# Performance work log

Measured on AMD Instinct MI355X. Metric: run time of the kernel, lower is better.

The kernel has to match this reference:

```python
import jax, jax.numpy as jnp
import numpy as np

N = 50000   # nodes
E = 800000  # edges (avg degree 16)
D = 96      # feature dim (in = hidden = out)


def setup_inputs() -> dict:
    key = jax.random.key(0)
    ks = jax.random.split(key, 6)
    scale = 1.0 / np.sqrt(D)
    return {
        "x": jax.random.normal(ks[0], (N, D), jnp.float32),
        "edge_index": jax.random.randint(ks[1], (2, E), 0, N, dtype=jnp.int64),
        "W1": jax.random.normal(ks[2], (D, D), jnp.float32) * scale,
        "b1": jnp.zeros((D,), jnp.float32),
        "a1": jnp.full((1,), 0.25, jnp.float32),  # PReLU weight
        "W2": jax.random.normal(ks[3], (D, D), jnp.float32) * scale,
        "b2": jnp.zeros((D,), jnp.float32),
    }


def _gcn_conv(x, W, b, src, dst, norm, n):
    # GCNConv: linear transform, then degree-normalized scatter-add aggregation
    h = x @ W                               # [N, D_out]
    msg = h[src] * norm[:, None]            # gather + scale, [E+N, D_out]
    out = jax.ops.segment_sum(msg, dst, num_segments=n)
    return out + b


def reference(x, edge_index, W1, b1, a1, W2, b2):
    n = x.shape[0]
    # add self loops (PyG gcn_norm default, fill_value=1.0)
    loop = jnp.arange(n, dtype=edge_index.dtype)
    src = jnp.concatenate([edge_index[0], loop])
    dst = jnp.concatenate([edge_index[1], loop])
    # symmetric normalization: D^{-1/2} A D^{-1/2}
    ones = jnp.ones(src.shape[0], dtype=x.dtype)
    deg = jax.ops.segment_sum(ones, dst, num_segments=n)
    dinv = jnp.where(deg > 0, jax.lax.rsqrt(deg), 0.0)
    norm = dinv[src] * dinv[dst]

    h = _gcn_conv(x, W1, b1, src, dst, norm, n)
    h = jnp.where(h > 0, h, a1 * h)  # PReLU (dropout p=0.0 is a no-op)
    h = _gcn_conv(h, W2, b2, src, dst, norm, n)
    return h
```

## Files before the change

kernel.cpp:

```cpp
#include <hip/hip_runtime.h>
#include <hip/hip_bf16.h>

#define NNODES 50000
#define NEDGES 800000
#define DIM    96
#define NBUCK  196
#define CAP    4608
#define TM     64
#define XPAD   104
#define PCH    3125

typedef __attribute__((ext_vector_type(8))) short   short8;
typedef __attribute__((ext_vector_type(4))) float   float4v;

__device__ __forceinline__ float loadF(const void* p, long i, int isbf) {
    return isbf ? __bfloat162float(((const __hip_bfloat16*)p)[i])
                : ((const float*)p)[i];
}
__device__ __forceinline__ int clampN(int v) {
    return v < 0 ? 0 : (v >= NNODES ? NNODES - 1 : v);
}
__device__ __forceinline__ int edgeDst(const int* w, int e, int is64) {
    return clampN(is64 ? w[2 * (NEDGES + e)] : w[NEDGES + e]);
}
__device__ __forceinline__ int edgeSrc(const int* w, int e, int is64) {
    return clampN(is64 ? w[2 * e] : w[e]);
}

__global__ void k_sniff(const unsigned* __restrict__ xw,
                        const unsigned* __restrict__ ew,
                        int* __restrict__ flags,
                        int* __restrict__ bcur) {
    int lane = threadIdx.x;
    for (int i = lane; i < NBUCK; i += 64) bcur[i] = 0;
    int bad = 0, nz = 0;
    for (int r = 0; r < 4; ++r) {
        unsigned w  = xw[lane + 64 * r];
        unsigned lo = w & 0xffffu;
        unsigned ex = (lo >> 7) & 0xffu;
        if (!(lo == 0u || (ex >= 90u && ex <= 145u))) bad++;
        unsigned o = ew[2 * (lane + 64 * r) + 1];
        if (o != 0u) nz++;
    }
    for (int off = 32; off; off >>= 1) {
        bad += __shfl_down(bad, off);
        nz  += __shfl_down(nz,  off);
    }
    if (lane == 0) {
        flags[0] = (bad <= 32) ? 1 : 0;
        flags[1] = (nz  <  4) ? 1 : 0;
    }
}

__global__ __launch_bounds__(256) void k_part(const int* __restrict__ w,
                                              int* __restrict__ bcur,
                                              unsigned* __restrict__ ebuf,
                                              const int* __restrict__ flags) {
    __shared__ unsigned pack[PCH];
    __shared__ int h[NBUCK];
    __shared__ int base[NBUCK];
    const int is64 = flags[1];
    const int tid  = threadIdx.x;
    const int e0   = blockIdx.x * PCH;

    for (int i = tid; i < NBUCK; i += 256) h[i] = 0;
    __syncthreads();
    for (int k = tid; k < PCH; k += 256) {
        int e = e0 + k;
        int s = edgeSrc(w, e, is64);
        int d = edgeDst(w, e, is64);
        pack[k] = ((unsigned)d << 16) | (unsigned)s;
        atomicAdd(&h[d >> 8], 1);
    }
    __syncthreads();
    for (int i = tid; i < NBUCK; i += 256) {
        int c = h[i];
        base[i] = c ? i * CAP + atomicAdd(&bcur[i], c) : 0;
        h[i] = 0;
    }
    __syncthreads();
    for (int k = tid; k < PCH; k += 256) {
        unsigned r = pack[k];
        int b = r >> 24;
        int pos = base[b] + atomicAdd(&h[b], 1);
        if (pos < (b + 1) * CAP) ebuf[pos] = r;
    }
}

__global__ __launch_bounds__(512) void k_csr(const unsigned* __restrict__ ebuf,
                                             const int* __restrict__ bcur,
                                             int* __restrict__ rowbeg,
                                             int* __restrict__ rowend,
                                             unsigned short* __restrict__ col,
                                             float* __restrict__ dinv) {
    __shared__ int h256[256];
    __shared__ int sc[256];
    __shared__ int cur[256];
    const int b   = blockIdx.x;
    const int tid = threadIdx.x;
    int cnt = bcur[b]; if (cnt > CAP) cnt = CAP;
    const int e0 = b * CAP;
    const int e1 = e0 + cnt;

    if (tid < 256) h256[tid] = 0;
    __syncthreads();
    for (int e = e0 + tid; e < e1; e += 512)
        atomicAdd(&h256[(ebuf[e] >> 16) & 255], 1);
    __syncthreads();
    int v = 0;
    if (tid < 256) { v = h256[tid]; sc[tid] = v; }
    __syncthreads();
    for (int off = 1; off < 256; off <<= 1) {
        int t2 = 0;
        if (tid < 256 && tid >= off) t2 = sc[tid - off];
        __syncthreads();
        if (tid < 256) sc[tid] += t2;
        __syncthreads();
    }
    if (tid < 256) {
        int start = e0 + sc[tid] - v;
        cur[tid] = start;
        int node = b * 256 + tid;
        if (node < NNODES) {
            rowbeg[node] = start;
            rowend[node] = start + v;
            dinv[node] = rsqrtf((float)v + 1.0f);
        }
    }
    __syncthreads();
    for (int e = e0 + tid; e < e1; e += 512) {
        unsigned r = ebuf[e];
        int pos = atomicAdd(&cur[(r >> 16) & 255], 1);
        col[pos] = (unsigned short)(r & 0xffffu);
    }
}

__global__ __launch_bounds__(256) void k_gemm_mfma(
        const void* __restrict__ X, int x_force_bf16,
        const void* __restrict__ W,
        const float* __restrict__ dinv,
        __hip_bfloat16* __restrict__ g,
        const int* __restrict__ flags) {
    __shared__ __hip_bfloat16 Xs[TM * XPAD];
    __shared__ __hip_bfloat16 Wt[DIM * XPAD];

    const int t    = threadIdx.x;
    const int fbf  = flags[0];
    const int xbf  = x_force_bf16 ? 1 : fbf;
    const int row0 = blockIdx.x * TM;

    if (!fbf) {
        const float4* Wv = (const float4*)W;
        for (int idx = t; idx < DIM * DIM / 4; idx += 256) {
            int k = idx / (DIM / 4);
            int n = (idx - k * (DIM / 4)) * 4;
            float4 w4 = Wv[idx];
            Wt[(n + 0) * XPAD + k] = __float2bfloat16(w4.x);
            Wt[(n + 1) * XPAD + k] = __float2bfloat16(w4.y);
            Wt[(n + 2) * XPAD + k] = __float2bfloat16(w4.z);
            Wt[(n + 3) * XPAD + k] = __float2bfloat16(w4.w);
        }
    } else {
        for (int idx = t; idx < DIM * DIM; idx += 256) {
            int k = idx / DIM, n = idx - k * DIM;
            Wt[n * XPAD + k] = __float2bfloat16(loadF(W, idx, 1));
        }
    }
    if (!xbf) {
        const float4* Xv = (const float4*)X;
        for (int idx = t; idx < TM * (DIM / 4); idx += 256) {
            int r = idx / (DIM / 4);
            int c = (idx - r * (DIM / 4)) * 4;
            int gr = row0 + r;
            float4 vv = {0.f, 0.f, 0.f, 0.f};
            if (gr < NNODES) vv = Xv[(size_t)gr * (DIM / 4) + (c >> 2)];
            *(__hip_bfloat162*)&Xs[r * XPAD + c] =
                __halves2bfloat162(__float2bfloat16(vv.x), __float2bfloat16(vv.y));
            *(__hip_bfloat162*)&Xs[r * XPAD + c + 2] =
                __halves2bfloat162(__float2bfloat16(vv.z), __float2bfloat16(vv.w));
        }
    } else {
        const short* Xs16 = (const short*)X;
        for (int idx = t; idx < TM * (DIM / 8); idx += 256) {
            int r  = idx / (DIM / 8);
            int c8 = idx - r * (DIM / 8);
            int gr = row0 + r;
            short8 vv = {0, 0, 0, 0, 0, 0, 0, 0};
            if (gr < NNODES) vv = *(const short8*)(Xs16 + (size_t)gr * DIM + c8 * 8);
            *(short8*)((short*)Xs + r * XPAD + c8 * 8) = vv;
        }
    }
    __syncthreads();

    const int wave = t >> 6;
    const int lane = t & 63;
    const int m    = lane & 15;
    const int quad = lane >> 4;

    const short* xsp = (const short*)Xs;
    short8 a[3];
#pragma unroll
    for (int kt = 0; kt < 3; ++kt)
        a[kt] = *(const short8*)(xsp + (wave * 16 + m) * XPAD + kt * 32 + quad * 8);

    float dv[4];
#pragma unroll
    for (int r2 = 0; r2 < 4; ++r2) {
        int gr = row0 + wave * 16 + quad * 4 + r2;
        dv[r2] = (gr < NNODES) ? dinv[gr] : 0.f;
    }

    const short* wtp = (const short*)Wt;
#pragma unroll
    for (int nt = 0; nt < 6; ++nt) {
        float4v acc = {0.f, 0.f, 0.f, 0.f};
#pragma unroll
        for (int kt = 0; kt < 3; ++kt) {
            short8 b = *(const short8*)(wtp + (nt * 16 + m) * XPAD + kt * 32 + quad * 8);
            acc = __builtin_amdgcn_mfma_f32_16x16x32_bf16(a[kt], b, acc, 0, 0, 0);
        }
#pragma unroll
        for (int r2 = 0; r2 < 4; ++r2) {
            int gr = row0 + wave * 16 + quad * 4 + r2;
            if (gr < NNODES)
                g[(size_t)gr * DIM + nt * 16 + m] = __float2bfloat16(acc[r2] * dv[r2]);
        }
    }
}

__global__ __launch_bounds__(256) void k_aggr(
        const __hip_bfloat16* __restrict__ g,
        const int* __restrict__ rowbeg,
        const int* __restrict__ rowend,
        const unsigned short* __restrict__ col,
        const float* __restrict__ dinv,
        const void* __restrict__ b,
        const void* __restrict__ a1,
        void* __restrict__ out,
        const int* __restrict__ flags, int prelu) {
    const int wave = threadIdx.x >> 6;
    const int lane = threadIdx.x & 63;
    const int row  = blockIdx.x * 4 + wave;
    if (row >= NNODES) return;
    const int fbf = flags[0];
    const __hip_bfloat162* gv = (const __hip_bfloat162*)g;
    const int c = lane;

    float2 acc = {0.f, 0.f};
    if (c < 48) acc = __bfloat1622float2(gv[(size_t)row * 48 + c]);

    const int p0 = rowbeg[row], p1 = rowend[row];
    int i = p0;
    for (; i + 16 <= p1; i += 16) {
        int s[16];
#pragma unroll
        for (int k = 0; k < 16; ++k) s[k] = col[i + k];
        if (c < 48) {
            float2 v[16];
#pragma unroll
            for (int k = 0; k < 16; ++k)
                v[k] = __bfloat1622float2(gv[(size_t)s[k] * 48 + c]);
            float2 t0, t1, t2, t3;
            t0.x = (v[0].x + v[1].x) + (v[2].x + v[3].x);
            t0.y = (v[0].y + v[1].y) + (v[2].y + v[3].y);
            t1.x = (v[4].x + v[5].x) + (v[6].x + v[7].x);
            t1.y = (v[4].y + v[5].y) + (v[6].y + v[7].y);
            t2.x = (v[8].x + v[9].x) + (v[10].x + v[11].x);
            t2.y = (v[8].y + v[9].y) + (v[10].y + v[11].y);
            t3.x = (v[12].x + v[13].x) + (v[14].x + v[15].x);
            t3.y = (v[12].y + v[13].y) + (v[14].y + v[15].y);
            acc.x += (t0.x + t1.x) + (t2.x + t3.x);
            acc.y += (t0.y + t1.y) + (t2.y + t3.y);
        }
    }
    for (; i + 8 <= p1; i += 8) {
        int s[8];
#pragma unroll
        for (int k = 0; k < 8; ++k) s[k] = col[i + k];
        if (c < 48) {
            float2 v[8];
#pragma unroll
            for (int k = 0; k < 8; ++k)
                v[k] = __bfloat1622float2(gv[(size_t)s[k] * 48 + c]);
            acc.x += ((v[0].x + v[1].x) + (v[2].x + v[3].x))
                   + ((v[4].x + v[5].x) + (v[6].x + v[7].x));
            acc.y += ((v[0].y + v[1].y) + (v[2].y + v[3].y))
                   + ((v[4].y + v[5].y) + (v[6].y + v[7].y));
        }
    }
    for (; i + 4 <= p1; i += 4) {
        int s0 = col[i], s1 = col[i+1], s2 = col[i+2], s3 = col[i+3];
        if (c < 48) {
            float2 v0 = __bfloat1622float2(gv[(size_t)s0 * 48 + c]);
            float2 v1 = __bfloat1622float2(gv[(size_t)s1 * 48 + c]);
            float2 v2 = __bfloat1622float2(gv[(size_t)s2 * 48 + c]);
            float2 v3 = __bfloat1622float2(gv[(size_t)s3 * 48 + c]);
            acc.x += (v0.x + v1.x) + (v2.x + v3.x);
            acc.y += (v0.y + v1.y) + (v2.y + v3.y);
        }
    }
    for (; i < p1; ++i) {
        int s = col[i];
        if (c < 48) {
            float2 v = __bfloat1622float2(gv[(size_t)s * 48 + c]);
            acc.x += v.x; acc.y += v.y;
        }
    }

    if (c < 48) {
        float dv = dinv[row];
        float vx = dv * acc.x + loadF(b, 2 * c,     fbf);
        float vy = dv * acc.y + loadF(b, 2 * c + 1, fbf);
        if (prelu) {
            float alpha = loadF(a1, 0, fbf);
            vx = vx > 0.f ? vx : alpha * vx;
            vy = vy > 0.f ? vy : alpha * vy;
            ((__hip_bfloat162*)out)[(size_t)row * 48 + c] =
                __halves2bfloat162(__float2bfloat16(vx), __float2bfloat16(vy));
        } else if (fbf) {
            ((__hip_bfloat162*)out)[(size_t)row * 48 + c] =
                __halves2bfloat162(__float2bfloat16(vx), __float2bfloat16(vy));
        } else {
            float2 o; o.x = vx; o.y = vy;
            ((float2*)out)[(size_t)row * 48 + c] = o;
        }
    }
}

extern "C" void kernel_launch(void* const* d_in, const int* in_sizes, int n_in,
                              void* d_out, int out_size, void* d_ws, size_t ws_size,
                              hipStream_t stream) {
    const void* x  = d_in[0];
    const int*  ei = (const int*)d_in[1];
    const void* W1 = d_in[2];
    const void* b1 = d_in[3];
    const void* a1 = d_in[4];
    const void* W2 = d_in[5];
    const void* b2 = d_in[6];

    size_t off = 0;
    auto alloc = [&](size_t bytes) { size_t p = off; off = (off + bytes + 255) & ~(size_t)255; return p; };
    char* ws = (char*)d_ws;
    int*            flags  = (int*)           (ws + alloc(1024));
    float*          dinv   = (float*)         (ws + alloc((size_t)NNODES * 4));
    int*            bcur   = (int*)           (ws + alloc((size_t)NBUCK * 4));
    int*            rowbeg = (int*)           (ws + alloc((size_t)NNODES * 4));
    int*            rowend = (int*)           (ws + alloc((size_t)NNODES * 4));
    unsigned*       ebuf   = (unsigned*)      (ws + alloc((size_t)NBUCK * CAP * 4));
    unsigned short* col    = (unsigned short*)(ws + alloc((size_t)NBUCK * CAP * 2));
    __hip_bfloat16* g      = (__hip_bfloat16*)(ws + alloc((size_t)NNODES * DIM * 2));
    __hip_bfloat16* g2     = (__hip_bfloat16*)(ws + alloc((size_t)NNODES * DIM * 2));
    if (ws_size < off) return;

    k_sniff<<<1, 64, 0, stream>>>((const unsigned*)x, (const unsigned*)ei, flags, bcur);
    k_part <<<256, 256, 0, stream>>>(ei, bcur, ebuf, flags);
    k_csr  <<<NBUCK, 512, 0, stream>>>(ebuf, bcur, rowbeg, rowend, col, dinv);

    const int gemm_grid = (NNODES + TM - 1) / TM;
    const int aggr_grid = (NNODES + 3) / 4;

    k_gemm_mfma<<<gemm_grid, 256, 0, stream>>>(x, 0, W1, dinv, g, flags);
    k_aggr<<<aggr_grid, 256, 0, stream>>>(g, rowbeg, rowend, col, dinv, b1, a1, g2, flags, 1);

    k_gemm_mfma<<<gemm_grid, 256, 0, stream>>>(g2, 1, W2, dinv, g, flags);
    k_aggr<<<aggr_grid, 256, 0, stream>>>(g, rowbeg, rowend, col, dinv, b2, a1, d_out, flags, 0);
}
```

Measured before the change: 204.0 us.

## Replace global bucket atomics with per-chunk local sort and histogram tables

The edge partition kernel now sorts each chunk's edges by bucket in shared memory and writes them contiguously, recording per-chunk bucket counts and offsets instead of using global atomic cursors into fixed-capacity buckets. The CSR kernel reads each bucket's pieces from all chunks through these tables, giving deterministic layout and coalesced writes in the partition step. The aggregation tail also replaces the 8/4/1 remainder loops with one clamped, masked 16-wide pass to cut branching. The cost is scattered short reads across 256 chunk segments in the CSR build and wasted gathers on padded tail lanes.

```diff
diff --git a/kernel.cpp b/kernel.cpp
--- a/kernel.cpp
+++ b/kernel.cpp
@@ -9,6 +9,8 @@
 #define TM     64
 #define XPAD   104
 #define PCH    3125
+#define NCHK   256
+#define HP     256
 
 typedef __attribute__((ext_vector_type(8))) short   short8;
 typedef __attribute__((ext_vector_type(4))) float   float4v;
@@ -20,19 +22,11 @@
 __device__ __forceinline__ int clampN(int v) {
     return v < 0 ? 0 : (v >= NNODES ? NNODES - 1 : v);
 }
-__device__ __forceinline__ int edgeDst(const int* w, int e, int is64) {
-    return clampN(is64 ? w[2 * (NEDGES + e)] : w[NEDGES + e]);
-}
-__device__ __forceinline__ int edgeSrc(const int* w, int e, int is64) {
-    return clampN(is64 ? w[2 * e] : w[e]);
-}
 
 __global__ void k_sniff(const unsigned* __restrict__ xw,
                         const unsigned* __restrict__ ew,
-                        int* __restrict__ flags,
-                        int* __restrict__ bcur) {
+                        int* __restrict__ flags) {
     int lane = threadIdx.x;
-    for (int i = lane; i < NBUCK; i += 64) bcur[i] = 0;
     int bad = 0, nz = 0;
     for (int r = 0; r < 4; ++r) {
         unsigned w  = xw[lane + 64 * r];
@@ -53,42 +47,65 @@
 }
 
 __global__ __launch_bounds__(256) void k_part(const int* __restrict__ w,
-                                              int* __restrict__ bcur,
-                                              unsigned* __restrict__ ebuf,
-                                              const int* __restrict__ flags) {
+                                              const int* __restrict__ flags,
+                                              int* __restrict__ hist,
+                                              int* __restrict__ hoff,
+                                              unsigned* __restrict__ ebuf) {
     __shared__ unsigned pack[PCH];
-    __shared__ int h[NBUCK];
-    __shared__ int base[NBUCK];
+    __shared__ unsigned opack[PCH];
+    __shared__ int h[256];
+    __shared__ int sc[256];
     const int is64 = flags[1];
-    const int tid  = threadIdx.x;
-    const int e0   = blockIdx.x * PCH;
-
-    for (int i = tid; i < NBUCK; i += 256) h[i] = 0;
-    __syncthreads();
-    for (int k = tid; k < PCH; k += 256) {
-        int e = e0 + k;
-        int s = edgeSrc(w, e, is64);
-        int d = edgeDst(w, e, is64);
-        pack[k] = ((unsigned)d << 16) | (unsigned)s;
-        atomicAdd(&h[d >> 8], 1);
-    }
-    __syncthreads();
-    for (int i = tid; i < NBUCK; i += 256) {
-        int c = h[i];
-        base[i] = c ? i * CAP + atomicAdd(&bcur[i], c) : 0;
-        h[i] = 0;
-    }
+    const int tid = threadIdx.x;
+    const int blk = blockIdx.x;
+    const int e0  = blk * PCH;
+
+    h[tid] = 0;
+    __syncthreads();
+    if (is64) {
+        const long long* wl = (const long long*)w;
+        for (int k = tid; k < PCH; k += 256) {
+            int s = clampN((int)wl[e0 + k]);
+            int d = clampN((int)wl[NEDGES + e0 + k]);
+            pack[k] = ((unsigned)d << 16) | (unsigned)s;
+            atomicAdd(&h[d >> 8], 1);
+        }
+    } else {
+        for (int k = tid; k < PCH; k += 256) {
+            int s = clampN(w[e0 + k]);
+            int d = clampN(w[NEDGES + e0 + k]);
+            pack[k] = ((unsigned)d << 16) | (unsigned)s;
+            atomicAdd(&h[d >> 8], 1);
+        }
+    }
+    __syncthreads();
+    int v = h[tid];
+    sc[tid] = v;
+    __syncthreads();
+    for (int off = 1; off < 256; off <<= 1) {
+        int t2 = (tid >= off) ? sc[tid - off] : 0;
+        __syncthreads();
+        sc[tid] += t2;
+        __syncthreads();
+    }
+    const int excl = sc[tid] - v;
+    hist[blk * HP + tid] = v;
+    hoff[blk * HP + tid] = excl;
+    h[tid] = excl;
     __syncthreads();
     for (int k = tid; k < PCH; k += 256) {
         unsigned r = pack[k];
-        int b = r >> 24;
-        int pos = base[b] + atomicAdd(&h[b], 1);
-        if (pos < (b + 1) * CAP) ebuf[pos] = r;
-    }
+        int pos = atomicAdd(&h[(r >> 16) >> 8], 1);
+        opack[pos] = r;
+    }
+    __syncthreads();
+    for (int k = tid; k < PCH; k += 256)
+        ebuf[e0 + k] = opack[k];
 }
 
 __global__ __launch_bounds__(512) void k_csr(const unsigned* __restrict__ ebuf,
-                                             const int* __restrict__ bcur,
+                                             const int* __restrict__ hist,
+                                             const int* __restrict__ hoff,
                                              int* __restrict__ rowbeg,
                                              int* __restrict__ rowend,
                                              unsigned short* __restrict__ col,
@@ -96,16 +113,25 @@
     __shared__ int h256[256];
     __shared__ int sc[256];
     __shared__ int cur[256];
+    __shared__ int scnt[256];
+    __shared__ int soff[256];
     const int b   = blockIdx.x;
     const int tid = threadIdx.x;
-    int cnt = bcur[b]; if (cnt > CAP) cnt = CAP;
-    const int e0 = b * CAP;
-    const int e1 = e0 + cnt;
-
-    if (tid < 256) h256[tid] = 0;
-    __syncthreads();
-    for (int e = e0 + tid; e < e1; e += 512)
-        atomicAdd(&h256[(ebuf[e] >> 16) & 255], 1);
+
+    if (tid < 256) {
+        scnt[tid] = hist[tid * HP + b];
+        soff[tid] = hoff[tid * HP + b];
+        h256[tid] = 0;
+    }
+    __syncthreads();
+    const int ch  = tid >> 1;
+    const int par = tid & 1;
+    {
+        const int cnt = scnt[ch];
+        const int off = ch * PCH + soff[ch];
+        for (int j = par; j < cnt; j += 2)
+            atomicAdd(&h256[(ebuf[off + j] >> 16) & 255], 1);
+    }
     __syncthreads();
     int v = 0;
     if (tid < 256) { v = h256[tid]; sc[tid] = v; }
@@ -118,7 +144,7 @@
         __syncthreads();
     }
     if (tid < 256) {
-        int start = e0 + sc[tid] - v;
+        int start = b * CAP + sc[tid] - v;
         cur[tid] = start;
         int node = b * 256 + tid;
         if (node < NNODES) {
@@ -128,10 +154,15 @@
         }
     }
     __syncthreads();
-    for (int e = e0 + tid; e < e1; e += 512) {
-        unsigned r = ebuf[e];
-        int pos = atomicAdd(&cur[(r >> 16) & 255], 1);
-        col[pos] = (unsigned short)(r & 0xffffu);
+    {
+        const int cnt = scnt[ch];
+        const int off = ch * PCH + soff[ch];
+        const int lim = (b + 1) * CAP;
+        for (int j = par; j < cnt; j += 2) {
+            unsigned r = ebuf[off + j];
+            int pos = atomicAdd(&cur[(r >> 16) & 255], 1);
+            if (pos < lim) col[pos] = (unsigned short)(r & 0xffffu);
+        }
     }
 }
 
@@ -273,37 +304,32 @@
             acc.y += (t0.y + t1.y) + (t2.y + t3.y);
         }
     }
-    for (; i + 8 <= p1; i += 8) {
-        int s[8];
-#pragma unroll
-        for (int k = 0; k < 8; ++k) s[k] = col[i + k];
+    if (i < p1) {
+        const int last = p1 - 1;
+        int s[16];
+#pragma unroll
+        for (int k = 0; k < 16; ++k) {
+            int idx = i + k;
+            s[k] = col[idx > last ? last : idx];
+        }
         if (c < 48) {
-            float2 v[8];
-#pragma unroll
-            for (int k = 0; k < 8; ++k)
+            float2 v[16];
+#pragma unroll
+            for (int k = 0; k < 16; ++k) {
                 v[k] = __bfloat1622float2(gv[(size_t)s[k] * 48 + c]);
-            acc.x += ((v[0].x + v[1].x) + (v[2].x + v[3].x))
-                   + ((v[4].x + v[5].x) + (v[6].x + v[7].x));
-            acc.y += ((v[0].y + v[1].y) + (v[2].y + v[3].y))
-                   + ((v[4].y + v[5].y) + (v[6].y + v[7].y));
-        }
-    }
-    for (; i + 4 <= p1; i += 4) {
-        int s0 = col[i], s1 = col[i+1], s2 = col[i+2], s3 = col[i+3];
-        if (c < 48) {
-            float2 v0 = __bfloat1622float2(gv[(size_t)s0 * 48 + c]);
-            float2 v1 = __bfloat1622float2(gv[(size_t)s1 * 48 + c]);
-            float2 v2 = __bfloat1622float2(gv[(size_t)s2 * 48 + c]);
-            float2 v3 = __bfloat1622float2(gv[(size_t)s3 * 48 + c]);
-            acc.x += (v0.x + v1.x) + (v2.x + v3.x);
-            acc.y += (v0.y + v1.y) + (v2.y + v3.y);
-        }
-    }
-    for (; i < p1; ++i) {
-        int s = col[i];
-        if (c < 48) {
-            float2 v = __bfloat1622float2(gv[(size_t)s * 48 + c]);
-            acc.x += v.x; acc.y += v.y;
+                if (i + k > last) { v[k].x = 0.f; v[k].y = 0.f; }
+            }
+            float2 t0, t1, t2, t3;
+            t0.x = (v[0].x + v[1].x) + (v[2].x + v[3].x);
+            t0.y = (v[0].y + v[1].y) + (v[2].y + v[3].y);
+            t1.x = (v[4].x + v[5].x) + (v[6].x + v[7].x);
+            t1.y = (v[4].y + v[5].y) + (v[6].y + v[7].y);
+            t2.x = (v[8].x + v[9].x) + (v[10].x + v[11].x);
+            t2.y = (v[8].y + v[9].y) + (v[10].y + v[11].y);
+            t3.x = (v[12].x + v[13].x) + (v[14].x + v[15].x);
+            t3.y = (v[12].y + v[13].y) + (v[14].y + v[15].y);
+            acc.x += (t0.x + t1.x) + (t2.x + t3.x);
+            acc.y += (t0.y + t1.y) + (t2.y + t3.y);
         }
     }
 
@@ -343,18 +369,19 @@
     char* ws = (char*)d_ws;
     int*            flags  = (int*)           (ws + alloc(1024));
     float*          dinv   = (float*)         (ws + alloc((size_t)NNODES * 4));
-    int*            bcur   = (int*)           (ws + alloc((size_t)NBUCK * 4));
     int*            rowbeg = (int*)           (ws + alloc((size_t)NNODES * 4));
     int*            rowend = (int*)           (ws + alloc((size_t)NNODES * 4));
-    unsigned*       ebuf   = (unsigned*)      (ws + alloc((size_t)NBUCK * CAP * 4));
-    unsigned short* col    = (unsigned short*)(ws + alloc((size_t)NBUCK * CAP * 2));
+    int*            hist   = (int*)           (ws + alloc((size_t)NCHK * HP * 4));
+    int*            hoff   = (int*)           (ws + alloc((size_t)NCHK * HP * 4));
+    unsigned*       ebuf   = (unsigned*)      (ws + alloc((size_t)NEDGES * 4));
+    unsigned short* col    = (unsigned short*)(ws + alloc((size_t)NBUCK * CAP * 2 + 256));
     __hip_bfloat16* g      = (__hip_bfloat16*)(ws + alloc((size_t)NNODES * DIM * 2));
     __hip_bfloat16* g2     = (__hip_bfloat16*)(ws + alloc((size_t)NNODES * DIM * 2));
     if (ws_size < off) return;
 
-    k_sniff<<<1, 64, 0, stream>>>((const unsigned*)x, (const unsigned*)ei, flags, bcur);
-    k_part <<<256, 256, 0, stream>>>(ei, bcur, ebuf, flags);
-    k_csr  <<<NBUCK, 512, 0, stream>>>(ebuf, bcur, rowbeg, rowend, col, dinv);
+    k_sniff<<<1, 64, 0, stream>>>((const unsigned*)x, (const unsigned*)ei, flags);
+    k_part <<<NCHK, 256, 0, stream>>>(ei, flags, hist, hoff, ebuf);
+    k_csr  <<<NBUCK, 512, 0, stream>>>(ebuf, hist, hoff, rowbeg, rowend, col, dinv);
 
     const int gemm_grid = (NNODES + TM - 1) / TM;
     const int aggr_grid = (NNODES + 3) / 4;
```

New measurement: 192.3 us. 1.06x faster.
